# Optimization experiments

Hardware: AMD Instinct MI355X
Metric: run time of the kernel (lower is better)

## Reference

```python
import jax, jax.numpy as jnp
import numpy as np

C = 512
CR = C // 8  # reduced channels for b/c projections


def setup_inputs() -> dict:
    key = jax.random.key(0)
    ks = jax.random.split(key, 7)
    scale = 1.0 / np.sqrt(C)
    x = jax.random.normal(ks[0], (4, C, 64, 64), dtype=jnp.float32)
    Wb = jax.random.normal(ks[1], (CR, C), dtype=jnp.float32) * scale
    bb = jax.random.normal(ks[2], (CR,), dtype=jnp.float32) * 0.01
    Wc = jax.random.normal(ks[3], (CR, C), dtype=jnp.float32) * scale
    bc = jax.random.normal(ks[4], (CR,), dtype=jnp.float32) * 0.01
    Wd = jax.random.normal(ks[5], (C, C), dtype=jnp.float32) * scale
    bd = jax.random.normal(ks[6], (C,), dtype=jnp.float32) * 0.01
    return {"x": x, "Wb": Wb, "bb": bb, "Wc": Wc, "bc": bc, "Wd": Wd, "bd": bd}


def reference(x, Wb, bb, Wc, bc, Wd, bd):
    B, Cc, H, W = x.shape
    N = H * W
    xf = x.reshape(B, Cc, N)  # [B, C, N] (1x1 conv == per-position matmul)
    b = jnp.einsum('kc,bcn->bkn', Wb, xf) + bb[None, :, None]  # [B, CR, N]
    c = jnp.einsum('kc,bcn->bkn', Wc, xf) + bc[None, :, None]  # [B, CR, N]
    d = jnp.einsum('kc,bcn->bkn', Wd, xf) + bd[None, :, None]  # [B, C, N]
    # s[b,i,j] = sum_k b[b,k,i] * c[b,k,j]; softmax over j
    s = jnp.einsum('bki,bkj->bij', b, c)  # [B, N, N]
    s = jax.nn.softmax(s, axis=-1)
    # torch.bmm(d, s): y[b,c,j] = sum_i d[b,c,i] * s[b,i,j]
    y = jnp.einsum('bci,bij->bcj', d, s)  # [B, C, N]
    return x + y.reshape(B, Cc, H, W)
```

## Files before the change

kernel.cpp:

```cpp
#include <hip/hip_runtime.h>
#include <hip/hip_bf16.h>

typedef float f32x4 __attribute__((ext_vector_type(4)));
typedef float f32x16 __attribute__((ext_vector_type(16)));
typedef short s16x8 __attribute__((ext_vector_type(8)));
typedef uint  u32x4 __attribute__((ext_vector_type(4)));

#define MFMA_BF16(a, b, c) __builtin_amdgcn_mfma_f32_16x16x32_bf16((a), (b), (c), 0, 0, 0)
#define MFMA32(a, b, c)    __builtin_amdgcn_mfma_f32_32x32x16_bf16((a), (b), (c), 0, 0, 0)

__device__ __forceinline__ ushort f2bf(float f) {
  uint u = __builtin_bit_cast(uint, f);
  u += 0x7FFFu + ((u >> 16) & 1u);
  return (ushort)(u >> 16);
}
__device__ __forceinline__ uint pack2bf(float a, float b) {
  return (uint)f2bf(a) | ((uint)f2bf(b) << 16);
}
__device__ __forceinline__ float pexp(float s) {
  float t = fmaf(s, 1.4426950408889634f, -43.2808512266689f);
  float r;
  asm("v_exp_f32 %0, %1" : "=v"(r) : "v"(t));
  return r;
}
__device__ __forceinline__ uint cvtpk(float lo, float hi) {
  uint r;
  asm("v_cvt_pk_bf16_f32 %0, %1, %2" : "=v"(r) : "v"(lo), "v"(hi));
  return r;
}
__device__ __forceinline__ void plswap(uint& a, uint& b) {
  asm("v_permlane32_swap_b32 %0, %1" : "+v"(a), "+v"(b));
}
__device__ __forceinline__ void gld16(const void* g, void* l) {
  __builtin_amdgcn_global_load_lds(
      (const __attribute__((address_space(1))) unsigned int*)g,
      (__attribute__((address_space(3))) unsigned int*)l, 16, 0, 0);
}

#define WS_XT    0UL
#define WS_D     16777216UL
#define WS_BT    33554432UL
#define WS_CT    35651584UL
#define WS_WCAT  37748736UL
#define WS_BCAT  38404096UL
#define WS_E     41943040UL
#define WS_E_NEED (WS_E + 134217728UL)

__global__ void k_prep_w(const float* __restrict__ Wb, const float* __restrict__ bb,
                         const float* __restrict__ Wc, const float* __restrict__ bc,
                         const float* __restrict__ Wd, const float* __restrict__ bd,
                         ushort* __restrict__ Wcat, float* __restrict__ bcat) {
  int idx = blockIdx.x * 256 + threadIdx.x;
  if (idx < 640 * 512) {
    int m = idx >> 9, k = idx & 511;
    float v = (m < 64) ? Wb[m * 512 + k] : (m < 128) ? Wc[(m - 64) * 512 + k] : Wd[(m - 128) * 512 + k];
    Wcat[idx] = f2bf(v);
  }
  if (idx < 640) {
    bcat[idx] = (idx < 64) ? bb[idx] : (idx < 128) ? bc[idx - 64] : bd[idx - 128];
  }
}

__global__ __launch_bounds__(256) void k_prep_xt(const float* __restrict__ x, ushort* __restrict__ xT) {
  __shared__ float tile[64][65];
  int bx = blockIdx.x;
  int b = bx >> 9;
  int c0 = ((bx >> 6) & 7) * 64;
  int n0 = (bx & 63) * 64;
  int t = threadIdx.x;
  const float* xb = x + (size_t)b * 512 * 4096;
#pragma unroll
  for (int p = 0; p < 4; ++p) {
    int cl = (t >> 4) + 16 * p;
    int nf = (t & 15) * 4;
    float4 v = *reinterpret_cast<const float4*>(xb + (size_t)(c0 + cl) * 4096 + n0 + nf);
    tile[cl][nf + 0] = v.x; tile[cl][nf + 1] = v.y; tile[cl][nf + 2] = v.z; tile[cl][nf + 3] = v.w;
  }
  __syncthreads();
  ushort* dst = xT + (size_t)b * 4096 * 512;
#pragma unroll
  for (int q = 0; q < 2; ++q) {
    int ch = t + 256 * q;
    int nl = ch >> 3;
    int cf = (ch & 7) * 8;
    uint4 o;
    o.x = pack2bf(tile[cf + 0][nl], tile[cf + 1][nl]);
    o.y = pack2bf(tile[cf + 2][nl], tile[cf + 3][nl]);
    o.z = pack2bf(tile[cf + 4][nl], tile[cf + 5][nl]);
    o.w = pack2bf(tile[cf + 6][nl], tile[cf + 7][nl]);
    *reinterpret_cast<uint4*>(dst + (size_t)(n0 + nl) * 512 + c0 + cf) = o;
  }
}

__global__ __launch_bounds__(256) void k_proj(const ushort* __restrict__ Wcat, const float* __restrict__ bcat,
                                              const ushort* __restrict__ xT, ushort* __restrict__ bT,
                                              ushort* __restrict__ cT, ushort* __restrict__ dmat) {
  int bx = blockIdx.x;
  int b = bx / 160;
  int r = bx % 160;
  int m0 = (r >> 5) * 128;
  int n0 = (r & 31) * 128;
  int t = threadIdx.x, l = t & 63, w = t >> 6;
  int wm = w >> 1, wn = w & 1, g = l >> 4, l15 = l & 15;
  const ushort* xb = xT + (size_t)b * 4096 * 512;
  f32x4 acc[4][4] = {};
  s16x8 bfn[4];
#pragma unroll
  for (int nt = 0; nt < 4; ++nt)
    bfn[nt] = *reinterpret_cast<const s16x8*>(xb + (size_t)(n0 + 64 * wn + 16 * nt + l15) * 512 + 8 * g);
  for (int k0 = 0; k0 < 512; k0 += 32) {
    s16x8 a[4], bf[4];
#pragma unroll
    for (int nt = 0; nt < 4; ++nt) bf[nt] = bfn[nt];
#pragma unroll
    for (int mt = 0; mt < 4; ++mt)
      a[mt] = *reinterpret_cast<const s16x8*>(Wcat + (size_t)(m0 + 64 * wm + 16 * mt + l15) * 512 + k0 + 8 * g);
    if (k0 + 32 < 512) {
#pragma unroll
      for (int nt = 0; nt < 4; ++nt)
        bfn[nt] = *reinterpret_cast<const s16x8*>(xb + (size_t)(n0 + 64 * wn + 16 * nt + l15) * 512 + k0 + 32 + 8 * g);
    }
    __builtin_amdgcn_sched_barrier(0);
#pragma unroll
    for (int mt = 0; mt < 4; ++mt)
#pragma unroll
      for (int nt = 0; nt < 4; ++nt)
        acc[mt][nt] = MFMA_BF16(a[mt], bf[nt], acc[mt][nt]);
  }
#pragma unroll
  for (int mt = 0; mt < 4; ++mt) {
    int mbase = m0 + 64 * wm + 16 * mt + 4 * g;
#pragma unroll
    for (int nt = 0; nt < 4; ++nt) {
      int n = n0 + 64 * wn + 16 * nt + l15;
      float vv[4];
      vv[0] = acc[mt][nt][0] + bcat[mbase + 0];
      vv[1] = acc[mt][nt][1] + bcat[mbase + 1];
      vv[2] = acc[mt][nt][2] + bcat[mbase + 2];
      vv[3] = acc[mt][nt][3] + bcat[mbase + 3];
      if (mbase < 64) {
        uint2 u2; u2.x = pack2bf(vv[0], vv[1]); u2.y = pack2bf(vv[2], vv[3]);
        size_t off = ((size_t)b * 4096 + n) * 64 + (size_t)((((mbase >> 3) ^ (n & 7)) << 3) + (mbase & 4));
        *reinterpret_cast<uint2*>(bT + off) = u2;
      } else if (mbase < 128) {
        uint2 u2; u2.x = pack2bf(vv[0], vv[1]); u2.y = pack2bf(vv[2], vv[3]);
        *reinterpret_cast<uint2*>(cT + ((size_t)b * 4096 + n) * 64 + (mbase - 64)) = u2;
      } else {
        int cc = mbase - 128;
        size_t fb = (((size_t)b * 256 + (n >> 4)) * 16) * 512;
#pragma unroll
        for (int rr = 0; rr < 4; ++rr) {
          int c = cc + rr;
          size_t idx = fb + (size_t)(c >> 5) * 512 + (size_t)(((n >> 3) & 1) * 32 + (c & 31)) * 8 + (n & 7);
          dmat[idx] = f2bf(vv[rr]);
        }
      }
    }
  }
}

__global__ __launch_bounds__(512) void k_stats_e(const ushort* __restrict__ bT, const ushort* __restrict__ cT,
                                                 ushort* __restrict__ dmat, ushort* __restrict__ E) {
  __shared__ ushort sCT[3][8192];
  __shared__ float lsum[64];
  int bx = blockIdx.x;
  int b = bx >> 6;
  int IC = bx & 63;
  int i0 = IC * 64;
  int t = threadIdx.x, w = t >> 6, l = t & 63;
  int l31 = l & 31, hi = l >> 5;
  int it_s = w & 1, Jl = w >> 1;
  if (t < 64) lsum[t] = 0.f;
  const ushort* bTb = bT + (size_t)b * 262144;
  const ushort* cTb = cT + (size_t)b * 262144;
  int ri = i0 + 32 * it_s + l31;
  int r7 = ri & 7;
  s16x8 af[4];
#pragma unroll
  for (int kc = 0; kc < 4; ++kc)
    af[kc] = *reinterpret_cast<const s16x8*>(bTb + (size_t)ri * 64 + (((2 * kc + hi) ^ r7) << 3));
  __builtin_amdgcn_sched_barrier(0);
  auto STAGE = [&](int st) {
#pragma unroll
    for (int q = 0; q < 2; ++q) {
      int idx = t + 512 * q;
      int row = idx >> 3, u = idx & 7;
      gld16(cTb + (size_t)(st * 128 + row) * 64 + ((u ^ (row & 7)) << 3), &sCT[st % 3][idx * 8]);
    }
  };
  STAGE(0); STAGE(1);
  asm volatile("s_waitcnt vmcnt(2)" ::: "memory");
  __syncthreads();

  f32x16 zero16;
#pragma unroll
  for (int r = 0; r < 16; ++r) zero16[r] = 0.f;
  float lacc[16];
#pragma unroll
  for (int r = 0; r < 16; ++r) lacc[r] = 0.f;

  for (int st = 0; st < 32; ++st) {
    if (st + 2 < 32) STAGE(st + 2);
    __builtin_amdgcn_sched_barrier(0);
    const ushort* cbuf = &sCT[st % 3][0];
    int rj = Jl * 32 + l31;
    int j7 = rj & 7;
    f32x16 sv = zero16;
    __builtin_amdgcn_s_setprio(1);
#pragma unroll
    for (int kc = 0; kc < 4; ++kc) {
      s16x8 cfv = *reinterpret_cast<const s16x8*>(cbuf + rj * 64 + (((2 * kc + hi) ^ j7) << 3));
      sv = MFMA32(af[kc], cfv, sv);
    }
    __builtin_amdgcn_s_setprio(0);
    float p[16];
#pragma unroll
    for (int r = 0; r < 16; ++r) { p[r] = pexp(sv[r]); lacc[r] += p[r]; }
    uint x0 = cvtpk(p[0], p[1]),   y0 = cvtpk(p[4], p[5]);
    uint x1 = cvtpk(p[2], p[3]),   y1 = cvtpk(p[6], p[7]);
    uint x2 = cvtpk(p[8], p[9]),   y2 = cvtpk(p[12], p[13]);
    uint x3 = cvtpk(p[10], p[11]), y3 = cvtpk(p[14], p[15]);
    plswap(x0, y0); plswap(x1, y1); plswap(x2, y2); plswap(x3, y3);
    u32x4 pw0 = {x0, x1, y0, y1};
    u32x4 pw1 = {x2, x3, y2, y3};
    int J = st * 4 + Jl;
    size_t fb = (((size_t)b * 64 + IC) * 128 + J) * 4 + 2 * it_s;
    *reinterpret_cast<u32x4*>(E + (fb * 64 + l) * 8)       = pw0;
    *reinterpret_cast<u32x4*>(E + ((fb + 1) * 64 + l) * 8) = pw1;
    asm volatile("s_waitcnt vmcnt(4)" ::: "memory");
    __builtin_amdgcn_s_barrier();
  }
#pragma unroll
  for (int off = 1; off < 32; off <<= 1)
#pragma unroll
    for (int r = 0; r < 16; ++r) lacc[r] += __shfl_xor(lacc[r], off);
  if (l31 == 0) {
#pragma unroll
    for (int r = 0; r < 16; ++r)
      atomicAdd(&lsum[32 * it_s + (r & 3) + 8 * (r >> 2) + 4 * hi], lacc[r]);
  }
  __syncthreads();
  if (t < 64) lsum[t] = 1.0f / fmaxf(lsum[t], 1e-30f);
  __syncthreads();
  int c = t;
  size_t rowb = (size_t)(c >> 5) * 512 + (size_t)(c & 31) * 8;
#pragma unroll
  for (int q = 0; q < 8; ++q) {
    int ic = (i0 >> 4) + (q >> 1);
    size_t idx = (((size_t)b * 256 + ic) * 16) * 512 + rowb + (size_t)(q & 1) * 256;
    s16x8 v = *reinterpret_cast<s16x8*>(dmat + idx);
    s16x8 nv;
#pragma unroll
    for (int e = 0; e < 8; ++e) {
      float f = __builtin_bit_cast(float, ((uint)(ushort)v[e]) << 16) * lsum[q * 8 + e];
      nv[e] = (short)f2bf(f);
    }
    *reinterpret_cast<s16x8*>(dmat + idx) = nv;
  }
}

__global__ __launch_bounds__(512, 2) void k_attn_e(const ushort* __restrict__ dmat, const ushort* __restrict__ E,
                                                   const float* __restrict__ x, float* __restrict__ out) {
  __shared__ ushort sE[2][8192];
  __shared__ ushort sD[2][8192];
  int bid = blockIdx.x;
  int gid = (bid & 7) * 64 + (bid >> 3);
  int b = gid >> 7, cb = (gid >> 5) & 3, jB = gid & 31;
  int t = threadIdx.x, w = t >> 6, l = t & 63;
  int l31 = l & 31, hi = l >> 5;
  int cg = w >> 1, jg = w & 1;
  f32x16 zero16;
#pragma unroll
  for (int r = 0; r < 16; ++r) zero16[r] = 0.f;
  f32x16 yacc[2];
  yacc[0] = zero16; yacc[1] = zero16;

  auto STAGE = [&](int buf, int it) {
    const ushort* ebase = E + ((((size_t)b * 64 + it) * 128 + jB * 4) * 4) * 512;
    const ushort* dbase = dmat + (((size_t)b * 256 + 4 * it) * 16 + cb * 4) * 512;
#pragma unroll
    for (int q = 0; q < 2; ++q) {
      int id = t + 512 * q;
      gld16(ebase + (size_t)id * 8, &sE[buf][id * 8]);
    }
#pragma unroll
    for (int q = 0; q < 2; ++q) {
      int id = t + 512 * q;
      gld16(dbase + (size_t)(id >> 8) * 8192 + (size_t)(id & 255) * 8, &sD[buf][id * 8]);
    }
  };

  STAGE(0, 0);
  asm volatile("s_waitcnt vmcnt(0)" ::: "memory");
  __builtin_amdgcn_s_barrier();
  __builtin_amdgcn_sched_barrier(0);

  int buf = 0;
  for (int it = 0; it < 64; ++it) {
    if (it + 1 < 64) STAGE(buf ^ 1, it + 1);
    __builtin_amdgcn_sched_barrier(0);
    const ushort* eb = &sE[buf][0];
    const ushort* db = &sD[buf][0];
    s16x8 dv[4];
#pragma unroll
    for (int ch = 0; ch < 4; ++ch)
      dv[ch] = *reinterpret_cast<const s16x8*>(db + ((ch * 4 + cg) * 64 + l) * 8);
    __builtin_amdgcn_s_setprio(1);
#pragma unroll
    for (int ch = 0; ch < 4; ++ch) {
#pragma unroll
      for (int jj = 0; jj < 2; ++jj) {
        s16x8 pfv = *reinterpret_cast<const s16x8*>(eb + (((2 * jg + jj) * 4 + ch) * 64 + l) * 8);
        yacc[jj] = MFMA32(dv[ch], pfv, yacc[jj]);
      }
    }
    __builtin_amdgcn_s_setprio(0);
    __builtin_amdgcn_sched_barrier(0);
    asm volatile("s_waitcnt vmcnt(0)" ::: "memory");
    __builtin_amdgcn_s_barrier();
    buf ^= 1;
  }
#pragma unroll
  for (int jj = 0; jj < 2; ++jj) {
#pragma unroll
    for (int r = 0; r < 16; ++r) {
      int row = cb * 128 + cg * 32 + (r & 3) + 8 * (r >> 2) + 4 * hi;
      int col = jB * 128 + (2 * jg + jj) * 32 + l31;
      size_t idx = ((size_t)b * 512 + row) * 4096 + col;
      out[idx] = x[idx] + yacc[jj][r];
    }
  }
}

__global__ __launch_bounds__(512) void k_stats_f(const ushort* __restrict__ bT, const ushort* __restrict__ cT,
                                                 ushort* __restrict__ dmat) {
  __shared__ ushort sCT[3][8192];
  __shared__ float lsum[64];
  int bx = blockIdx.x;
  int b = bx >> 6;
  int i0 = (bx & 63) * 64;
  int t = threadIdx.x, l = t & 63, w = t >> 6;
  int wm = w >> 1, wn = w & 1, g = l >> 4, l15 = l & 15;
  if (t < 64) lsum[t] = 0.f;
  const ushort* bTb = bT + (size_t)b * 262144;
  const ushort* cTb = cT + (size_t)b * 262144;
  int arow = i0 + 16 * wm + l15;
  int r7 = arow & 7;
  const ushort* abase = bTb + (size_t)arow * 64;
  s16x8 a0 = *reinterpret_cast<const s16x8*>(abase + ((g ^ r7) << 3));
  s16x8 a1 = *reinterpret_cast<const s16x8*>(abase + (((g + 4) ^ r7) << 3));
  auto STAGE = [&](int jt) {
#pragma unroll
    for (int q = 0; q < 2; ++q) {
      int idx = t + 512 * q;
      int row = idx >> 3, u = idx & 7;
      gld16(cTb + (size_t)(jt * 128 + row) * 64 + ((u ^ (row & 7)) << 3), &sCT[jt % 3][idx * 8]);
    }
  };
  STAGE(0); STAGE(1);
  asm volatile("s_waitcnt vmcnt(2)" ::: "memory");
  __syncthreads();
  float lacc[4] = {0.f, 0.f, 0.f, 0.f};
  for (int jt = 0; jt < 32; ++jt) {
    if (jt + 2 < 32) STAGE(jt + 2);
    __builtin_amdgcn_sched_barrier(0);
    const ushort* cbuf = &sCT[jt % 3][0];
#pragma unroll
    for (int nt = 0; nt < 4; ++nt) {
      int row = 64 * wn + 16 * nt + l15;
      int rs = row & 7;
      s16x8 b0 = *reinterpret_cast<const s16x8*>(cbuf + row * 64 + ((g ^ rs) << 3));
      s16x8 b1 = *reinterpret_cast<const s16x8*>(cbuf + row * 64 + (((g + 4) ^ rs) << 3));
      f32x4 s = {0.f, 0.f, 0.f, 0.f};
      s = MFMA_BF16(a0, b0, s);
      s = MFMA_BF16(a1, b1, s);
#pragma unroll
      for (int rr = 0; rr < 4; ++rr) lacc[rr] += pexp(s[rr]);
    }
    if (jt < 30) { asm volatile("s_waitcnt vmcnt(2)" ::: "memory"); }
    else         { asm volatile("s_waitcnt vmcnt(0)" ::: "memory"); }
    __builtin_amdgcn_s_barrier();
  }
#pragma unroll
  for (int off = 1; off < 16; off <<= 1)
#pragma unroll
    for (int rr = 0; rr < 4; ++rr) lacc[rr] += __shfl_xor(lacc[rr], off);
  if (l15 == 0) {
#pragma unroll
    for (int rr = 0; rr < 4; ++rr) atomicAdd(&lsum[16 * wm + 4 * g + rr], lacc[rr]);
  }
  __syncthreads();
  if (t < 64) lsum[t] = 1.0f / fmaxf(lsum[t], 1e-30f);
  __syncthreads();
  int c = t;
  size_t rowb = (size_t)(c >> 5) * 512 + (size_t)(c & 31) * 8;
#pragma unroll
  for (int q = 0; q < 8; ++q) {
    int ic = (i0 >> 4) + (q >> 1);
    size_t idx = (((size_t)b * 256 + ic) * 16) * 512 + rowb + (size_t)(q & 1) * 256;
    s16x8 v = *reinterpret_cast<s16x8*>(dmat + idx);
    s16x8 nv;
#pragma unroll
    for (int e = 0; e < 8; ++e) {
      float f = __builtin_bit_cast(float, ((uint)(ushort)v[e]) << 16) * lsum[q * 8 + e];
      nv[e] = (short)f2bf(f);
    }
    *reinterpret_cast<s16x8*>(dmat + idx) = nv;
  }
}

__global__ __launch_bounds__(512, 2) void k_attn_f(const ushort* __restrict__ bT, const ushort* __restrict__ cT,
                                                   const ushort* __restrict__ dmat,
                                                   const float* __restrict__ x, float* __restrict__ out) {
  __shared__ ushort sBT[3][4096];
  __shared__ ushort sP[2][8192];
  int bid = blockIdx.x;
  int gid = (bid & 7) * 64 + (bid >> 3);
  int b   = gid >> 7;
  int cb  = (gid >> 5) & 3;
  int jB  = gid & 31;
  int t = threadIdx.x, w = t >> 6, l = t & 63;
  int l31 = l & 31, hi = l >> 5;
  int it_s = w >> 2, jt_s = w & 3;
  int cg = w >> 1, jg = w & 1;
  const ushort* bTb = bT + (size_t)b * 262144;
  const ushort* cTb = cT + (size_t)b * 262144;
  int js = jB * 128 + jt_s * 32 + l31;
  s16x8 cf[4];
#pragma unroll
  for (int kc = 0; kc < 4; ++kc)
    cf[kc] = *reinterpret_cast<const s16x8*>(cTb + (size_t)js * 64 + kc * 16 + hi * 8);
  int ctg = cb * 4 + cg;
  f32x16 zero16;
#pragma unroll
  for (int r = 0; r < 16; ++r) zero16[r] = 0.f;
  f32x16 yacc[2];
  yacc[0] = zero16; yacc[1] = zero16;
  auto STAGE = [&](int it) {
    gld16(bTb + (size_t)it * 4096 + (size_t)t * 8, &sBT[it % 3][t * 8]);
  };
  STAGE(0); STAGE(1);
  asm volatile("s_waitcnt vmcnt(1)" ::: "memory");
  __builtin_amdgcn_s_barrier();
  __builtin_amdgcn_sched_barrier(0);
  for (int it = 0; it < 64; ++it) {
    s16x8 dv[4];
#pragma unroll
    for (int ch = 0; ch < 4; ++ch)
      dv[ch] = *reinterpret_cast<const s16x8*>(
          dmat + ((((size_t)b * 256 + (4 * it + ch)) * 16 + ctg) * 64 + l) * 8);
    if (it + 2 < 64) STAGE(it + 2);
    __builtin_amdgcn_sched_barrier(0);
    const ushort* bbuf = &sBT[it % 3][0];
    f32x16 sv = zero16;
    __builtin_amdgcn_s_setprio(1);
#pragma unroll
    for (int kc = 0; kc < 4; ++kc) {
      const s16x8 bfv = *reinterpret_cast<const s16x8*>(
          bbuf + (32 * it_s + l31) * 64 + (((2 * kc + hi) ^ (l31 & 7)) << 3));
      sv = MFMA32(bfv, cf[kc], sv);
    }
    __builtin_amdgcn_s_setprio(0);
    float p[16];
#pragma unroll
    for (int r = 0; r < 16; ++r) p[r] = pexp(sv[r]);
    uint x0 = cvtpk(p[0], p[1]),   y0 = cvtpk(p[4], p[5]);
    uint x1 = cvtpk(p[2], p[3]),   y1 = cvtpk(p[6], p[7]);
    uint x2 = cvtpk(p[8], p[9]),   y2 = cvtpk(p[12], p[13]);
    uint x3 = cvtpk(p[10], p[11]), y3 = cvtpk(p[14], p[15]);
    plswap(x0, y0); plswap(x1, y1); plswap(x2, y2); plswap(x3, y3);
    u32x4 pw0 = {x0, x1, y0, y1};
    u32x4 pw1 = {x2, x3, y2, y3};
    ushort* pbuf = &sP[it & 1][0];
    int fi0 = jt_s * 4 + 2 * it_s;
    *reinterpret_cast<s16x8*>(pbuf + (fi0 * 64 + l) * 8)       = __builtin_bit_cast(s16x8, pw0);
    *reinterpret_cast<s16x8*>(pbuf + ((fi0 + 1) * 64 + l) * 8) = __builtin_bit_cast(s16x8, pw1);
    asm volatile("s_waitcnt lgkmcnt(0)" ::: "memory");
    __builtin_amdgcn_s_barrier();
    if (it < 62) { asm volatile("s_waitcnt vmcnt(1)" ::: "memory"); }
    else         { asm volatile("s_waitcnt vmcnt(0)" ::: "memory"); }
    __builtin_amdgcn_sched_barrier(0);
    __builtin_amdgcn_s_setprio(1);
#pragma unroll
    for (int ch = 0; ch < 4; ++ch) {
#pragma unroll
      for (int jj = 0; jj < 2; ++jj) {
        int jt = 2 * jg + jj;
        const s16x8 pfv = *reinterpret_cast<const s16x8*>(pbuf + ((jt * 4 + ch) * 64 + l) * 8);
        yacc[jj] = MFMA32(dv[ch], pfv, yacc[jj]);
      }
    }
    __builtin_amdgcn_s_setprio(0);
  }
#pragma unroll
  for (int jj = 0; jj < 2; ++jj) {
#pragma unroll
    for (int r = 0; r < 16; ++r) {
      int row = cb * 128 + cg * 32 + (r & 3) + 8 * (r >> 2) + 4 * hi;
      int col = jB * 128 + (2 * jg + jj) * 32 + l31;
      size_t idx = ((size_t)b * 512 + row) * 4096 + col;
      out[idx] = x[idx] + yacc[jj][r];
    }
  }
}

extern "C" void kernel_launch(void* const* d_in, const int* in_sizes, int n_in,
                              void* d_out, int out_size, void* d_ws, size_t ws_size,
                              hipStream_t stream) {
  const float* x  = (const float*)d_in[0];
  const float* Wb = (const float*)d_in[1];
  const float* bb = (const float*)d_in[2];
  const float* Wc = (const float*)d_in[3];
  const float* bc = (const float*)d_in[4];
  const float* Wd = (const float*)d_in[5];
  const float* bd = (const float*)d_in[6];
  char* ws = (char*)d_ws;
  ushort* xT   = (ushort*)(ws + WS_XT);
  ushort* dmat = (ushort*)(ws + WS_D);
  ushort* bT   = (ushort*)(ws + WS_BT);
  ushort* cT   = (ushort*)(ws + WS_CT);
  ushort* Wcat = (ushort*)(ws + WS_WCAT);
  float*  bcat = (float*)(ws + WS_BCAT);
  ushort* E    = (ushort*)(ws + WS_E);
  float*  out  = (float*)d_out;

  k_prep_w<<<1280, 256, 0, stream>>>(Wb, bb, Wc, bc, Wd, bd, Wcat, bcat);
  k_prep_xt<<<2048, 256, 0, stream>>>(x, xT);
  k_proj<<<640, 256, 0, stream>>>(Wcat, bcat, xT, bT, cT, dmat);
  if (ws_size >= WS_E_NEED) {
    k_stats_e<<<256, 512, 0, stream>>>(bT, cT, dmat, E);
    k_attn_e<<<512, 512, 0, stream>>>(dmat, E, x, out);
  } else {
    k_stats_f<<<256, 512, 0, stream>>>(bT, cT, dmat);
    k_attn_f<<<512, 512, 0, stream>>>(bT, cT, dmat, x, out);
  }
}
```

Measured before the change: 186.0 us.

## Enlarge k_attn_e output tile to 256 channels and triple-buffer loads

Each block of the D·E attention-apply kernel now covers 256 output channels instead of 128, using a 2x2 grid of MFMA accumulators per wave. Each E tile loaded into shared memory is therefore reused across twice as many channels, and the grid shrinks from 512 to 256 blocks. Staging moves from double to triple buffering with a partial vmcnt wait, so the loads for iteration it+2 stay in flight while iteration it computes. In exchange the kernel uses more registers and LDS, drops the two-blocks-per-CU launch bound, and with 256 blocks may only about fill the CUs once, which lowers occupancy.

```diff
diff --git a/kernel.cpp b/kernel.cpp
--- a/kernel.cpp
+++ b/kernel.cpp
@@ -259,75 +259,85 @@
   }
 }
 
-__global__ __launch_bounds__(512, 2) void k_attn_e(const ushort* __restrict__ dmat, const ushort* __restrict__ E,
-                                                   const float* __restrict__ x, float* __restrict__ out) {
-  __shared__ ushort sE[2][8192];
-  __shared__ ushort sD[2][8192];
+__global__ __launch_bounds__(512) void k_attn_e(const ushort* __restrict__ dmat, const ushort* __restrict__ E,
+                                                const float* __restrict__ x, float* __restrict__ out) {
+  __shared__ ushort sE[3][8192];
+  __shared__ ushort sD[3][16384];
   int bid = blockIdx.x;
-  int gid = (bid & 7) * 64 + (bid >> 3);
-  int b = gid >> 7, cb = (gid >> 5) & 3, jB = gid & 31;
+  int gid = (bid & 7) * 32 + (bid >> 3);
+  int b = gid >> 6, jB = (gid >> 1) & 31, cb2 = gid & 1;
   int t = threadIdx.x, w = t >> 6, l = t & 63;
   int l31 = l & 31, hi = l >> 5;
   int cg = w >> 1, jg = w & 1;
   f32x16 zero16;
 #pragma unroll
   for (int r = 0; r < 16; ++r) zero16[r] = 0.f;
-  f32x16 yacc[2];
-  yacc[0] = zero16; yacc[1] = zero16;
-
-  auto STAGE = [&](int buf, int it) {
+  f32x16 yacc[2][2];
+  yacc[0][0] = zero16; yacc[0][1] = zero16; yacc[1][0] = zero16; yacc[1][1] = zero16;
+
+  auto STAGE = [&](int it) {
+    int buf = it % 3;
     const ushort* ebase = E + ((((size_t)b * 64 + it) * 128 + jB * 4) * 4) * 512;
-    const ushort* dbase = dmat + (((size_t)b * 256 + 4 * it) * 16 + cb * 4) * 512;
 #pragma unroll
     for (int q = 0; q < 2; ++q) {
       int id = t + 512 * q;
       gld16(ebase + (size_t)id * 8, &sE[buf][id * 8]);
     }
 #pragma unroll
-    for (int q = 0; q < 2; ++q) {
-      int id = t + 512 * q;
-      gld16(dbase + (size_t)(id >> 8) * 8192 + (size_t)(id & 255) * 8, &sD[buf][id * 8]);
+    for (int q = 0; q < 4; ++q) {
+      const ushort* dch = dmat + (((size_t)b * 256 + 4 * it + q) * 16 + cb2 * 8) * 512;
+      gld16(dch + (size_t)t * 8, &sD[buf][(q * 512 + t) * 8]);
     }
   };
 
-  STAGE(0, 0);
-  asm volatile("s_waitcnt vmcnt(0)" ::: "memory");
+  STAGE(0); STAGE(1);
+  asm volatile("s_waitcnt vmcnt(6)" ::: "memory");
   __builtin_amdgcn_s_barrier();
   __builtin_amdgcn_sched_barrier(0);
 
-  int buf = 0;
   for (int it = 0; it < 64; ++it) {
-    if (it + 1 < 64) STAGE(buf ^ 1, it + 1);
-    __builtin_amdgcn_sched_barrier(0);
-    const ushort* eb = &sE[buf][0];
-    const ushort* db = &sD[buf][0];
-    s16x8 dv[4];
-#pragma unroll
-    for (int ch = 0; ch < 4; ++ch)
-      dv[ch] = *reinterpret_cast<const s16x8*>(db + ((ch * 4 + cg) * 64 + l) * 8);
+    if (it + 2 < 64) STAGE(it + 2);
+    __builtin_amdgcn_sched_barrier(0);
+    const ushort* eb = &sE[it % 3][0];
+    const ushort* db = &sD[it % 3][0];
+    s16x8 dv[2][4], pfv[2][4];
+#pragma unroll
+    for (int ch = 0; ch < 4; ++ch) {
+#pragma unroll
+      for (int ct = 0; ct < 2; ++ct)
+        dv[ct][ch] = *reinterpret_cast<const s16x8*>(db + ((ch * 8 + cg * 2 + ct) * 512 + l * 8));
+#pragma unroll
+      for (int jj = 0; jj < 2; ++jj)
+        pfv[jj][ch] = *reinterpret_cast<const s16x8*>(eb + (((jg * 2 + jj) * 4 + ch) * 512 + l * 8));
+    }
     __builtin_amdgcn_s_setprio(1);
 #pragma unroll
     for (int ch = 0; ch < 4; ++ch) {
 #pragma unroll
-      for (int jj = 0; jj < 2; ++jj) {
-        s16x8 pfv = *reinterpret_cast<const s16x8*>(eb + (((2 * jg + jj) * 4 + ch) * 64 + l) * 8);
-        yacc[jj] = MFMA32(dv[ch], pfv, yacc[jj]);
+      for (int ct = 0; ct < 2; ++ct)
+#pragma unroll
+        for (int jj = 0; jj < 2; ++jj)
+          yacc[ct][jj] = MFMA32(dv[ct][ch], pfv[jj][ch], yacc[ct][jj]);
+    }
+    __builtin_amdgcn_s_setprio(0);
+    __builtin_amdgcn_sched_barrier(0);
+    if (it < 62) { asm volatile("s_waitcnt vmcnt(6)" ::: "memory"); }
+    else         { asm volatile("s_waitcnt vmcnt(0)" ::: "memory"); }
+    __builtin_amdgcn_s_barrier();
+    __builtin_amdgcn_sched_barrier(0);
+  }
+
+#pragma unroll
+  for (int ct = 0; ct < 2; ++ct) {
+#pragma unroll
+    for (int jj = 0; jj < 2; ++jj) {
+#pragma unroll
+      for (int r = 0; r < 16; ++r) {
+        int row = cb2 * 256 + cg * 64 + ct * 32 + (r & 3) + 8 * (r >> 2) + 4 * hi;
+        int col = jB * 128 + (jg * 2 + jj) * 32 + l31;
+        size_t idx = ((size_t)b * 512 + row) * 4096 + col;
+        out[idx] = x[idx] + yacc[ct][jj][r];
       }
-    }
-    __builtin_amdgcn_s_setprio(0);
-    __builtin_amdgcn_sched_barrier(0);
-    asm volatile("s_waitcnt vmcnt(0)" ::: "memory");
-    __builtin_amdgcn_s_barrier();
-    buf ^= 1;
-  }
-#pragma unroll
-  for (int jj = 0; jj < 2; ++jj) {
-#pragma unroll
-    for (int r = 0; r < 16; ++r) {
-      int row = cb * 128 + cg * 32 + (r & 3) + 8 * (r >> 2) + 4 * hi;
-      int col = jB * 128 + (2 * jg + jj) * 32 + l31;
-      size_t idx = ((size_t)b * 512 + row) * 4096 + col;
-      out[idx] = x[idx] + yacc[jj][r];
     }
   }
 }
@@ -529,7 +539,7 @@
   k_proj<<<640, 256, 0, stream>>>(Wcat, bcat, xT, bT, cT, dmat);
   if (ws_size >= WS_E_NEED) {
     k_stats_e<<<256, 512, 0, stream>>>(bT, cT, dmat, E);
-    k_attn_e<<<512, 512, 0, stream>>>(dmat, E, x, out);
+    k_attn_e<<<256, 512, 0, stream>>>(dmat, E, x, out);
   } else {
     k_stats_f<<<256, 512, 0, stream>>>(bT, cT, dmat);
     k_attn_f<<<512, 512, 0, stream>>>(bT, cT, dmat, x, out);
```

Result: slower. 190.0 us (+2.1%).

## Load D operand straight to registers and triple-buffer E with prefetch distance two

Applied to the files above, without the earlier changes.

The attention-output kernel no longer stages the D matrix through LDS; each wave loads its D fragments directly from global memory into registers. The E tiles move to a three-slot LDS ring filled two iterations ahead, and all E fragments are read from LDS before a partial vmcnt wait and the MFMA block. The aim is to cut LDS traffic and footprint and hide global latency better. In exchange, D is loaded redundantly by the two waves that share a channel group, and correctness now depends on careful vmcnt counting.

```diff
diff --git a/kernel.cpp b/kernel.cpp
--- a/kernel.cpp
+++ b/kernel.cpp
@@ -261,65 +261,65 @@
 
 __global__ __launch_bounds__(512, 2) void k_attn_e(const ushort* __restrict__ dmat, const ushort* __restrict__ E,
                                                    const float* __restrict__ x, float* __restrict__ out) {
-  __shared__ ushort sE[2][8192];
-  __shared__ ushort sD[2][8192];
+  __shared__ ushort sE[3][8192];
   int bid = blockIdx.x;
   int gid = (bid & 7) * 64 + (bid >> 3);
   int b = gid >> 7, cb = (gid >> 5) & 3, jB = gid & 31;
   int t = threadIdx.x, w = t >> 6, l = t & 63;
   int l31 = l & 31, hi = l >> 5;
   int cg = w >> 1, jg = w & 1;
+  int ctg = cb * 4 + cg;
   f32x16 zero16;
 #pragma unroll
   for (int r = 0; r < 16; ++r) zero16[r] = 0.f;
   f32x16 yacc[2];
   yacc[0] = zero16; yacc[1] = zero16;
 
-  auto STAGE = [&](int buf, int it) {
+  auto STAGE = [&](int it) {
     const ushort* ebase = E + ((((size_t)b * 64 + it) * 128 + jB * 4) * 4) * 512;
-    const ushort* dbase = dmat + (((size_t)b * 256 + 4 * it) * 16 + cb * 4) * 512;
 #pragma unroll
     for (int q = 0; q < 2; ++q) {
       int id = t + 512 * q;
-      gld16(ebase + (size_t)id * 8, &sE[buf][id * 8]);
-    }
-#pragma unroll
-    for (int q = 0; q < 2; ++q) {
-      int id = t + 512 * q;
-      gld16(dbase + (size_t)(id >> 8) * 8192 + (size_t)(id & 255) * 8, &sD[buf][id * 8]);
+      gld16(ebase + (size_t)id * 8, &sE[it % 3][id * 8]);
     }
   };
 
-  STAGE(0, 0);
-  asm volatile("s_waitcnt vmcnt(0)" ::: "memory");
+  STAGE(0); STAGE(1);
+  asm volatile("s_waitcnt vmcnt(2)" ::: "memory");
   __builtin_amdgcn_s_barrier();
   __builtin_amdgcn_sched_barrier(0);
 
-  int buf = 0;
   for (int it = 0; it < 64; ++it) {
-    if (it + 1 < 64) STAGE(buf ^ 1, it + 1);
-    __builtin_amdgcn_sched_barrier(0);
-    const ushort* eb = &sE[buf][0];
-    const ushort* db = &sD[buf][0];
     s16x8 dv[4];
 #pragma unroll
     for (int ch = 0; ch < 4; ++ch)
-      dv[ch] = *reinterpret_cast<const s16x8*>(db + ((ch * 4 + cg) * 64 + l) * 8);
+      dv[ch] = *reinterpret_cast<const s16x8*>(
+          dmat + ((((size_t)b * 256 + (4 * it + ch)) * 16 + ctg) * 64 + l) * 8);
+    __builtin_amdgcn_sched_barrier(0);
+    if (it + 2 < 64) STAGE(it + 2);
+    __builtin_amdgcn_sched_barrier(0);
+    const ushort* eb = &sE[it % 3][0];
+    s16x8 pfv[2][4];
+#pragma unroll
+    for (int jj = 0; jj < 2; ++jj)
+#pragma unroll
+      for (int ch = 0; ch < 4; ++ch)
+        pfv[jj][ch] = *reinterpret_cast<const s16x8*>(
+            eb + (((2 * jg + jj) * 4 + ch) * 64 + l) * 8);
+    __builtin_amdgcn_sched_barrier(0);
+    if (it < 62) { asm volatile("s_waitcnt vmcnt(2)" ::: "memory"); }
+    else         { asm volatile("s_waitcnt vmcnt(0)" ::: "memory"); }
+    __builtin_amdgcn_sched_barrier(0);
     __builtin_amdgcn_s_setprio(1);
 #pragma unroll
     for (int ch = 0; ch < 4; ++ch) {
-#pragma unroll
-      for (int jj = 0; jj < 2; ++jj) {
-        s16x8 pfv = *reinterpret_cast<const s16x8*>(eb + (((2 * jg + jj) * 4 + ch) * 64 + l) * 8);
-        yacc[jj] = MFMA32(dv[ch], pfv, yacc[jj]);
-      }
+      yacc[0] = MFMA32(dv[ch], pfv[0][ch], yacc[0]);
+      yacc[1] = MFMA32(dv[ch], pfv[1][ch], yacc[1]);
     }
     __builtin_amdgcn_s_setprio(0);
-    __builtin_amdgcn_sched_barrier(0);
-    asm volatile("s_waitcnt vmcnt(0)" ::: "memory");
     __builtin_amdgcn_s_barrier();
-    buf ^= 1;
-  }
+  }
+
 #pragma unroll
   for (int jj = 0; jj < 2; ++jj) {
 #pragma unroll
```

Measured after the change: 194.3 us. 4.5% more time.
